# Kernel optimization log

Measured on AMD Instinct MI355X. Metric: run time of the kernel, lower is better.

The kernel has to match this reference:

```python
import jax, jax.numpy as jnp
import numpy as np

NEG_SLOPE = 0.1  # LeakyReLU slope used throughout CamLiFlow

def _batch_gather(feat, idx):
    # feat: [B, C, N], idx: [B, N, K] -> [B, C, N, K]
    return jax.vmap(lambda f, i: f[:, i])(feat, idx)

def _point_conv(xyz, feat, idx, wn_w, wn_b, lin_w, lin_b):
    # xyz: [B,3,N], feat: [B,C,N], idx: [B,N,K]
    B, _, N = xyz.shape
    feat_cat = jnp.concatenate([xyz, feat], axis=1)            # [B, C+3, N]
    knn_xyz = _batch_gather(xyz, idx)                          # [B, 3, N, K]
    rel = knn_xyz - xyz[:, :, :, None]                         # centered neighbor coords
    # weight net: 1x1 conv 3 -> 8 + LeakyReLU
    w = jax.nn.leaky_relu(
        jnp.einsum('oc,bcnk->bonk', wn_w, rel) + wn_b[None, :, None, None],
        NEG_SLOPE)                                             # [B, 8, N, K]
    knn_feat = _batch_gather(feat_cat, idx)                    # [B, C+3, N, K]
    agg = jnp.einsum('bonk,bcnk->bnoc', w, knn_feat)           # [B, N, 8, C+3]
    out = agg.reshape(B, N, -1) @ lin_w.T + lin_b              # [B, N, out]
    return jax.nn.leaky_relu(out, NEG_SLOPE).transpose(0, 2, 1)  # [B, out, N]

def _conv1d(x, w, b):
    # 1x1 Conv1d: x [B,C,N], w [O,C], b [O]
    return jnp.einsum('oc,bcn->bon', w, x) + b[None, :, None]

def setup_inputs() -> dict:
    key = jax.random.key(0)
    ks = jax.random.split(key, 16)
    B, N, K = 4, 8192, 16
    C0, C1, C2, C3 = 128, 128, 128, 64
    s = 0.02
    inp = {
        'xyz': jax.random.normal(ks[0], (B, 3, N), jnp.float32),
        'feat': jax.random.normal(ks[1], (B, C0, N), jnp.float32),
        'knn_indices': jax.random.randint(ks[2], (B, N, K), 0, N),
        # point_conv1
        'wn1_w': jax.random.normal(ks[3], (8, 3), jnp.float32) * s,
        'wn1_b': jnp.zeros((8,), jnp.float32),
        'lin1_w': jax.random.normal(ks[4], (C1, 8 * (C0 + 3)), jnp.float32) * s,
        'lin1_b': jnp.zeros((C1,), jnp.float32),
        # point_conv2
        'wn2_w': jax.random.normal(ks[5], (8, 3), jnp.float32) * s,
        'wn2_b': jnp.zeros((8,), jnp.float32),
        'lin2_w': jax.random.normal(ks[6], (C2, 8 * (C1 + 3)), jnp.float32) * s,
        'lin2_b': jnp.zeros((C2,), jnp.float32),
        # MLP1d: C2 -> C2 -> C3 (1x1 convs + LeakyReLU)
        'm1_w': jax.random.normal(ks[7], (C2, C2), jnp.float32) * s,
        'm1_b': jnp.zeros((C2,), jnp.float32),
        'm2_w': jax.random.normal(ks[8], (C3, C2), jnp.float32) * s,
        'm2_b': jnp.zeros((C3,), jnp.float32),
        # conv_last: C3 -> 3
        'cl_w': jax.random.normal(ks[9], (3, C3), jnp.float32) * s,
        'cl_b': jnp.zeros((3,), jnp.float32),
    }
    return inp

def reference(xyz, feat, knn_indices, wn1_w, wn1_b, lin1_w, lin1_b,
              wn2_w, wn2_b, lin2_w, lin2_b, m1_w, m1_b, m2_w, m2_b,
              cl_w, cl_b):
    f = _point_conv(xyz, feat, knn_indices, wn1_w, wn1_b, lin1_w, lin1_b)  # [B,128,N]
    f = _point_conv(xyz, f, knn_indices, wn2_w, wn2_b, lin2_w, lin2_b)     # [B,128,N]
    f = jax.nn.leaky_relu(_conv1d(f, m1_w, m1_b), NEG_SLOPE)
    flow_feat = jax.nn.leaky_relu(_conv1d(f, m2_w, m2_b), NEG_SLOPE)       # [B,64,N]
    flow = _conv1d(flow_feat, cl_w, cl_b)                                  # [B,3,N]
    return flow_feat, flow
```

## Files before the change

kernel.cpp:

```cpp
#include <hip/hip_runtime.h>

typedef __bf16 bf16x8 __attribute__((ext_vector_type(8)));
typedef float  f32x4  __attribute__((ext_vector_type(4)));
typedef float  f32x2  __attribute__((ext_vector_type(2)));
typedef unsigned int u32x4 __attribute__((ext_vector_type(4)));
typedef unsigned short u16;

#define NPTS 8192
#define NB   4
#define KNN  16
#define ROW  136
#define CF   131
#define JBLK 136
#define NSTEP 34
#define AGG_STRIDE 1096
#define HALF_U16 8704
#define WOFF  17408
#define RBOFF 19456
#define SMEM_U16 19712
#define F2T   0
#define H1OFF 2304
#define FFOFF 4608
#define NEG 0.1f

#define WAITVM(n) __builtin_amdgcn_s_waitcnt(0x0F70 | (n))
#define SB() __builtin_amdgcn_sched_barrier(0)

__device__ __forceinline__ float b2f(u16 h) {
    return __uint_as_float(((unsigned int)h) << 16);
}
__device__ __forceinline__ u16 f2bf(float f) {
    unsigned int u = __float_as_uint(f);
    return (u16)((u + 0x8000u) >> 16);
}
__device__ __forceinline__ void dma16(const u16* g, u16* l) {
    __builtin_amdgcn_global_load_lds(
        (const __attribute__((address_space(1))) void*)g,
        (__attribute__((address_space(3))) void*)l, 16, 0, 0);
}
__device__ __forceinline__ float lrelu(float v) {
    return (v < 0.0f) ? NEG * v : v;
}

__global__ __launch_bounds__(256) void pack_all(
    const float* __restrict__ xyz, const float* __restrict__ feat,
    u16* __restrict__ fcT1, u16* __restrict__ fcT2, float* __restrict__ xyzF,
    const float* __restrict__ l1, const float* __restrict__ l2,
    const float* __restrict__ w1, const float* __restrict__ w2,
    u16* __restrict__ o1, u16* __restrict__ o2,
    u16* __restrict__ o3, u16* __restrict__ o4)
{
    int t = threadIdx.x;
    if (blockIdx.x < 512) {
        __shared__ u16 tile[CF * 65];
        int blk = blockIdx.x;
        int b = blk >> 7;
        int n0 = (blk & 127) << 6;
        int nn = t & 63;
        #pragma unroll 1
        for (int c = (t >> 6); c < CF; c += 4) {
            float v;
            if (c < 3) v = xyz[(size_t)b * 3 * NPTS + (size_t)c * NPTS + n0 + nn];
            else       v = feat[(size_t)b * 128 * NPTS + (size_t)(c - 3) * NPTS + n0 + nn];
            tile[c * 65 + nn] = f2bf(v);
            if (c < 3) xyzF[((size_t)b * NPTS + n0 + nn) * 4 + c] = v;
        }
        __syncthreads();
        #pragma unroll 1
        for (int e = t; e < 64 * ROW; e += 256) {
            int r = e / ROW;
            int c = e - r * ROW;
            u16 v = (c < CF) ? tile[c * 65 + r] : (u16)0;
            size_t row = (size_t)b * NPTS + n0 + r;
            fcT1[row * ROW + c] = v;
            if (c < 3 || c >= CF) fcT2[row * ROW + c] = v;
        }
    } else {
        int blk = blockIdx.x - 512;
        const float* w; u16* out; int O, Cin, remap, b0;
        if (blk < 68)       { w = l1; out = o1; O = 128; Cin = 1048; remap = 1; b0 = 0; }
        else if (blk < 136) { w = l2; out = o2; O = 128; Cin = 1048; remap = 1; b0 = 68; }
        else if (blk < 144) { w = w1; out = o3; O = 128; Cin = 128;  remap = 0; b0 = 136; }
        else                { w = w2; out = o4; O = 64;  Cin = 128;  remap = 0; b0 = 144; }
        int T = O >> 4;
        int tid = (blk - b0) * 256 + t;
        int l = tid & 63;
        int st = tid >> 6;
        int tt = st % T;
        int s = st / T;
        int o = tt * 16 + (l & 15);
        int kb = s * 32 + ((l >> 4) * 8);
        #pragma unroll 1
        for (int j = 0; j < 8; j++) {
            int kh = kb + j;
            u16 v = 0;
            if (remap) {
                int jj = kh / JBLK, cc = kh - jj * JBLK;
                if (cc < CF) v = f2bf(w[(size_t)o * Cin + jj * CF + cc]);
            } else {
                if (kh < Cin) v = f2bf(w[(size_t)o * Cin + kh]);
            }
            out[(size_t)tid * 8 + j] = v;
        }
    }
}

__device__ __forceinline__ void pc_core(
    u16* __restrict__ smem,
    const u16* __restrict__ fcT, const float* __restrict__ xyzF,
    const int* __restrict__ knn, const float* __restrict__ wn_w,
    const float* __restrict__ wn_b, const u16* __restrict__ lwP,
    int pt0, int b, int n0, f32x4& acc1o, f32x4& acc2o)
{
    int t = threadIdx.x;
    int wv = t >> 6, lane = t & 63;
    int p = t >> 4, cl = t & 15;
    u16* rb16 = smem + RBOFF;

    {
        size_t rowC = (size_t)b * NPTS + n0 + p;
        int idxv = knn[rowC * KNN + cl];
        int rb = b * NPTS + idxv;
        rb16[p * 16 + cl] = (u16)rb;
        f32x4 cx = *(const f32x4*)(xyzF + rowC * 4);
        f32x4 nx = *(const f32x4*)(xyzF + (size_t)rb * 4);
        float rx = nx[0] - cx[0], ry = nx[1] - cx[1], rz = nx[2] - cx[2];
        unsigned int wp[4];
        #pragma unroll
        for (int jj = 0; jj < 4; jj++) {
            float a0 = lrelu(wn_w[(2 * jj) * 3 + 0] * rx + wn_w[(2 * jj) * 3 + 1] * ry +
                             wn_w[(2 * jj) * 3 + 2] * rz + wn_b[2 * jj]);
            float a1 = lrelu(wn_w[(2 * jj + 1) * 3 + 0] * rx + wn_w[(2 * jj + 1) * 3 + 1] * ry +
                             wn_w[(2 * jj + 1) * 3 + 2] * rz + wn_b[2 * jj + 1]);
            wp[jj] = (unsigned)f2bf(a0) | ((unsigned)f2bf(a1) << 16);
        }
        *(u32x4*)(smem + WOFF + (p * 16 + cl) * 8) = (u32x4){wp[0], wp[1], wp[2], wp[3]};
    }

    f32x2 acc[4][8];
    float acct[8];
    #pragma unroll
    for (int i = 0; i < 4; i++)
        #pragma unroll
        for (int j = 0; j < 8; j++) acc[i][j] = (f32x2){0.f, 0.f};
    #pragma unroll
    for (int j = 0; j < 8; j++) acct[j] = 0.f;

    int rbidx[5], remu[5], ldso[5];
    #pragma unroll
    for (int i = 0; i < 5; i++) {
        int slot = i * 64 + lane;
        int rl = slot / 17;
        int rem = slot - rl * 17;
        int pp = wv * 4 + (rl >> 2);
        int kk = rl & 3;
        rbidx[i] = pp * 16 + kk;
        remu[i] = rem * 8;
        ldso[i] = (pp * 4 + kk) * 136 + rem * 8;
    }

    auto issue = [&](int c) {
        int h = c & 1;
        #pragma unroll
        for (int i = 0; i < 5; i++) {
            if (i < 4 || lane < 16) {
                int rb = (int)rb16[rbidx[i] + c * 4];
                dma16(fcT + (size_t)rb * ROW + remu[i],
                      smem + h * HALF_U16 + ldso[i]);
            }
        }
    };
    auto consume = [&](int c) {
        int h = c & 1;
        const u16* rpb = smem + h * HALF_U16 + p * (4 * 136);
        const u16* wpb = smem + WOFF + (p * 16 + c * 4) * 8;
        #pragma unroll 2
        for (int kk = 0; kk < 4; kk++) {
            u32x4 rv = *(const u32x4*)(rpb + kk * 136 + cl * 8);
            float tl = (cl < 3) ? b2f(rpb[kk * 136 + 128 + cl]) : 0.0f;
            u32x4 wv4 = *(const u32x4*)(wpb + kk * 8);
            f32x2 v[4];
            float wr[8];
            #pragma unroll
            for (int i = 0; i < 4; i++) {
                unsigned int u = rv[i];
                v[i] = (f32x2){__uint_as_float(u << 16),
                               __uint_as_float(u & 0xFFFF0000u)};
                unsigned int uw = wv4[i];
                wr[2 * i]     = __uint_as_float(uw << 16);
                wr[2 * i + 1] = __uint_as_float(uw & 0xFFFF0000u);
            }
            #pragma unroll
            for (int j = 0; j < 8; j++) {
                f32x2 w2 = (f32x2){wr[j], wr[j]};
                #pragma unroll
                for (int i = 0; i < 4; i++) acc[i][j] += v[i] * w2;
                acct[j] += tl * wr[j];
            }
        }
    };

    issue(0); issue(1);
    #pragma unroll 1
    for (int c = 0; c < 2; c++) {
        WAITVM(5); SB(); consume(c); SB(); issue(c + 2); SB();
    }
    WAITVM(5); SB(); consume(2); SB();
    WAITVM(0); SB(); consume(3);
    __syncthreads();

    {
        #pragma unroll
        for (int j = 0; j < 8; j++) {
            unsigned int o[4];
            #pragma unroll
            for (int i = 0; i < 4; i++) {
                unsigned int lo = f2bf(acc[i][j].x);
                unsigned int hi = f2bf(acc[i][j].y);
                o[i] = lo | (hi << 16);
            }
            *(u32x4*)(smem + p * AGG_STRIDE + j * JBLK + cl * 8) =
                (u32x4){o[0], o[1], o[2], o[3]};
        }
        if (cl < 3) {
            #pragma unroll
            for (int j = 0; j < 8; j++)
                smem[p * AGG_STRIDE + j * JBLK + 128 + cl] = f2bf(acct[j]);
        }
        if (cl < 5) {
            #pragma unroll
            for (int j = 0; j < 8; j++)
                smem[p * AGG_STRIDE + j * JBLK + CF + cl] = 0;
        }
    }
    __syncthreads();

    {
        int m = lane & 15, quad = lane >> 4;
        f32x4 a1 = {0.f, 0.f, 0.f, 0.f};
        f32x4 a2 = {0.f, 0.f, 0.f, 0.f};
        #pragma unroll 4
        for (int s = 0; s < NSTEP; s++) {
            u32x4 av = *(const u32x4*)(smem + m * AGG_STRIDE + s * 32 + quad * 8);
            u32x4 bv1 = *(const u32x4*)(lwP + (((size_t)(s * 8 + wv) * 64 + lane) << 3));
            u32x4 bv2 = *(const u32x4*)(lwP + (((size_t)(s * 8 + wv + 4) * 64 + lane) << 3));
            a1 = __builtin_amdgcn_mfma_f32_16x16x32_bf16(
                __builtin_bit_cast(bf16x8, av), __builtin_bit_cast(bf16x8, bv1), a1, 0, 0, 0);
            a2 = __builtin_amdgcn_mfma_f32_16x16x32_bf16(
                __builtin_bit_cast(bf16x8, av), __builtin_bit_cast(bf16x8, bv2), a2, 0, 0, 0);
        }
        acc1o = a1; acc2o = a2;
    }
}

__global__ __launch_bounds__(256) void pc_kernel0(
    const u16* __restrict__ fcT, const float* __restrict__ xyzF,
    const int* __restrict__ knn, const float* __restrict__ wn_w,
    const float* __restrict__ wn_b, const u16* __restrict__ lwP,
    const float* __restrict__ lin_b, u16* __restrict__ out)
{
    __shared__ __align__(16) u16 smem[SMEM_U16];
    int t = threadIdx.x;
    int wv = t >> 6, lane = t & 63;
    int pt0 = blockIdx.x * 16;
    int b = pt0 >> 13;
    int n0 = pt0 & (NPTS - 1);
    f32x4 a1, a2;
    pc_core(smem, fcT, xyzF, knn, wn_w, wn_b, lwP, pt0, b, n0, a1, a2);
    int col = lane & 15, quad = lane >> 4;
    int o1 = wv * 16 + col, o2 = (wv + 4) * 16 + col;
    float bb1 = lin_b[o1], bb2 = lin_b[o2];
    #pragma unroll
    for (int r = 0; r < 4; r++) {
        int prow = pt0 + quad * 4 + r;
        out[(size_t)prow * ROW + 3 + o1] = f2bf(lrelu(a1[r] + bb1));
        out[(size_t)prow * ROW + 3 + o2] = f2bf(lrelu(a2[r] + bb2));
    }
}

__global__ __launch_bounds__(256) void pc_kernel1(
    const u16* __restrict__ fcT, const float* __restrict__ xyzF,
    const int* __restrict__ knn, const float* __restrict__ wn_w,
    const float* __restrict__ wn_b, const u16* __restrict__ lwP,
    const float* __restrict__ lin_b,
    const u16* __restrict__ m1P, const float* __restrict__ m1_b,
    const u16* __restrict__ m2P, const float* __restrict__ m2_b,
    const float* __restrict__ cl_w, const float* __restrict__ cl_b,
    float* __restrict__ dout)
{
    __shared__ __align__(16) u16 smem[SMEM_U16];
    int t = threadIdx.x;
    int wv = t >> 6, lane = t & 63;
    int pt0 = blockIdx.x * 16;
    int b = pt0 >> 13;
    int n0 = pt0 & (NPTS - 1);
    f32x4 a1, a2;
    pc_core(smem, fcT, xyzF, knn, wn_w, wn_b, lwP, pt0, b, n0, a1, a2);
    int col = lane & 15, quad = lane >> 4;
    int m = lane & 15;

    {
        int o1 = wv * 16 + col, o2 = (wv + 4) * 16 + col;
        float bb1 = lin_b[o1], bb2 = lin_b[o2];
        __syncthreads();
        #pragma unroll
        for (int r = 0; r < 4; r++) {
            int pr = quad * 4 + r;
            smem[F2T + pr * 128 + o1] = f2bf(lrelu(a1[r] + bb1));
            smem[F2T + pr * 128 + o2] = f2bf(lrelu(a2[r] + bb2));
        }
    }
    __syncthreads();

    {
        f32x4 g1 = {0.f, 0.f, 0.f, 0.f};
        f32x4 g2 = {0.f, 0.f, 0.f, 0.f};
        #pragma unroll 2
        for (int s = 0; s < 4; s++) {
            u32x4 av = *(const u32x4*)(smem + F2T + m * 128 + s * 32 + quad * 8);
            u32x4 bv1 = *(const u32x4*)(m1P + (((size_t)(s * 8 + wv) * 64 + lane) << 3));
            u32x4 bv2 = *(const u32x4*)(m1P + (((size_t)(s * 8 + wv + 4) * 64 + lane) << 3));
            g1 = __builtin_amdgcn_mfma_f32_16x16x32_bf16(
                __builtin_bit_cast(bf16x8, av), __builtin_bit_cast(bf16x8, bv1), g1, 0, 0, 0);
            g2 = __builtin_amdgcn_mfma_f32_16x16x32_bf16(
                __builtin_bit_cast(bf16x8, av), __builtin_bit_cast(bf16x8, bv2), g2, 0, 0, 0);
        }
        int o1 = wv * 16 + col, o2 = (wv + 4) * 16 + col;
        float bb1 = m1_b[o1], bb2 = m1_b[o2];
        #pragma unroll
        for (int r = 0; r < 4; r++) {
            int pr = quad * 4 + r;
            smem[H1OFF + pr * 136 + o1] = f2bf(lrelu(g1[r] + bb1));
            smem[H1OFF + pr * 136 + o2] = f2bf(lrelu(g2[r] + bb2));
        }
    }
    __syncthreads();

    {
        float* ffp = (float*)(smem + FFOFF);
        f32x4 g = {0.f, 0.f, 0.f, 0.f};
        #pragma unroll 2
        for (int s = 0; s < 4; s++) {
            u32x4 av = *(const u32x4*)(smem + H1OFF + m * 136 + s * 32 + quad * 8);
            u32x4 bv = *(const u32x4*)(m2P + (((size_t)(s * 4 + wv) * 64 + lane) << 3));
            g = __builtin_amdgcn_mfma_f32_16x16x32_bf16(
                __builtin_bit_cast(bf16x8, av), __builtin_bit_cast(bf16x8, bv), g, 0, 0, 0);
        }
        int o = wv * 16 + col;
        float bb = m2_b[o];
        #pragma unroll
        for (int r = 0; r < 4; r++) {
            int pr = quad * 4 + r;
            float v = lrelu(g[r] + bb);
            dout[((size_t)b * 64 + o) * NPTS + n0 + pr] = v;
            ffp[pr * 68 + o] = v;
        }
    }
    __syncthreads();

    if (t < 48) {
        float* ffp = (float*)(smem + FFOFF);
        int pp = t & 15, oo = t >> 4;
        float a = cl_b[oo];
        #pragma unroll 8
        for (int i = 0; i < 64; i++)
            a += cl_w[oo * 64 + i] * ffp[pp * 68 + i];
        dout[(size_t)NB * 64 * NPTS + ((size_t)b * 3 + oo) * NPTS + n0 + pp] = a;
    }
}

extern "C" void kernel_launch(void* const* d_in, const int* in_sizes, int n_in,
                              void* d_out, int out_size, void* d_ws, size_t ws_size,
                              hipStream_t stream) {
    const float* xyz   = (const float*)d_in[0];
    const float* feat  = (const float*)d_in[1];
    const int*   knn   = (const int*)d_in[2];
    const float* wn1_w = (const float*)d_in[3];
    const float* wn1_b = (const float*)d_in[4];
    const float* lin1w = (const float*)d_in[5];
    const float* lin1b = (const float*)d_in[6];
    const float* wn2_w = (const float*)d_in[7];
    const float* wn2_b = (const float*)d_in[8];
    const float* lin2w = (const float*)d_in[9];
    const float* lin2b = (const float*)d_in[10];
    const float* m1_w  = (const float*)d_in[11];
    const float* m1_b  = (const float*)d_in[12];
    const float* m2_w  = (const float*)d_in[13];
    const float* m2_b  = (const float*)d_in[14];
    const float* cl_w  = (const float*)d_in[15];
    const float* cl_b  = (const float*)d_in[16];
    float* out = (float*)d_out;

    char* ws = (char*)d_ws;
    const size_t BN = (size_t)NB * NPTS;
    u16*   fcT1 = (u16*)(ws);
    u16*   fcT2 = (u16*)(ws + 8912896);
    float* xyzF = (float*)(ws + 17825792);
    u16*   lw1P = (u16*)(ws + 18350080);
    u16*   lw2P = (u16*)(ws + 18628608);
    u16*   m1P  = (u16*)(ws + 18907136);
    u16*   m2P  = (u16*)(ws + 18939904);

    (void)in_sizes; (void)n_in; (void)out_size; (void)ws_size;

    pack_all<<<dim3(660), dim3(256), 0, stream>>>(
        xyz, feat, fcT1, fcT2, xyzF,
        lin1w, lin2w, m1_w, m2_w, lw1P, lw2P, m1P, m2P);
    pc_kernel0<<<dim3(BN / 16), dim3(256), 0, stream>>>(
        fcT1, xyzF, knn, wn1_w, wn1_b, lw1P, lin1b, fcT2);
    pc_kernel1<<<dim3(BN / 16), dim3(256), 0, stream>>>(
        fcT2, xyzF, knn, wn2_w, wn2_b, lw2P, lin2b,
        m1P, m1_b, m2P, m2_b, cl_w, cl_b, out);
}
```

Baseline: 194.3 us.

## Shrink LDS footprint with c-major aggregate layout and chunked staging

Reorders the aggregated K dimension from j-major (136-padded blocks per weight channel) to channel-major interleaved (c*8+j), with the packed linear weights remapped to match. The aggregate is written to LDS in four 32-channel groups plus a tail, each followed by the MFMA steps for that slice, instead of staging the full 16x1096 tile at once. Neighbor gather chunks shrink from 4 to 2 neighbors with 8 pipeline stages, which halves the double buffer. Together these roughly halve shared memory per block, likely to raise occupancy, at the cost of several extra __syncthreads in the projection phase. The F2T row stride is also padded to 136 to reduce bank conflicts.

```diff
diff --git a/kernel.cpp b/kernel.cpp
--- a/kernel.cpp
+++ b/kernel.cpp
@@ -11,13 +11,12 @@
 #define KNN  16
 #define ROW  136
 #define CF   131
-#define JBLK 136
 #define NSTEP 34
-#define AGG_STRIDE 1096
-#define HALF_U16 8704
-#define WOFF  17408
-#define RBOFF 19456
-#define SMEM_U16 19712
+#define HALF_U16 4352
+#define WOFF  8704
+#define RBOFF 10752
+#define SMEM_U16 11008
+#define AGB_STRIDE 264
 #define F2T   0
 #define H1OFF 2304
 #define FFOFF 4608
@@ -95,7 +94,7 @@
             int kh = kb + j;
             u16 v = 0;
             if (remap) {
-                int jj = kh / JBLK, cc = kh - jj * JBLK;
+                int cc = kh >> 3, jj = kh & 7;
                 if (cc < CF) v = f2bf(w[(size_t)o * Cin + jj * CF + cc]);
             } else {
                 if (kh < Cin) v = f2bf(w[(size_t)o * Cin + kh]);
@@ -146,36 +145,37 @@
     #pragma unroll
     for (int j = 0; j < 8; j++) acct[j] = 0.f;
 
-    int rbidx[5], remu[5], ldso[5];
+    int rbidx[3], remu[3], ldso[3];
     #pragma unroll
-    for (int i = 0; i < 5; i++) {
+    for (int i = 0; i < 3; i++) {
         int slot = i * 64 + lane;
         int rl = slot / 17;
         int rem = slot - rl * 17;
-        int pp = wv * 4 + (rl >> 2);
-        int kk = rl & 3;
+        int pp = wv * 4 + (rl >> 1);
+        int kk = rl & 1;
         rbidx[i] = pp * 16 + kk;
         remu[i] = rem * 8;
-        ldso[i] = (pp * 4 + kk) * 136 + rem * 8;
+        ldso[i] = wv * 1088 + rl * 136 + rem * 8;
     }
 
     auto issue = [&](int c) {
         int h = c & 1;
         #pragma unroll
-        for (int i = 0; i < 5; i++) {
-            if (i < 4 || lane < 16) {
-                int rb = (int)rb16[rbidx[i] + c * 4];
+        for (int i = 0; i < 3; i++) {
+            if (i < 2 || lane < 8) {
+                int rb = (int)rb16[rbidx[i] + c * 2];
                 dma16(fcT + (size_t)rb * ROW + remu[i],
                       smem + h * HALF_U16 + ldso[i]);
             }
         }
     };
+
     auto consume = [&](int c) {
         int h = c & 1;
-        const u16* rpb = smem + h * HALF_U16 + p * (4 * 136);
-        const u16* wpb = smem + WOFF + (p * 16 + c * 4) * 8;
-        #pragma unroll 2
-        for (int kk = 0; kk < 4; kk++) {
+        const u16* rpb = smem + h * HALF_U16 + p * 272;
+        const u16* wpb = smem + WOFF + (p * 16 + c * 2) * 8;
+        #pragma unroll
+        for (int kk = 0; kk < 2; kk++) {
             u32x4 rv = *(const u32x4*)(rpb + kk * 136 + cl * 8);
             float tl = (cl < 3) ? b2f(rpb[kk * 136 + 128 + cl]) : 0.0f;
             u32x4 wv4 = *(const u32x4*)(wpb + kk * 8);
@@ -202,46 +202,67 @@
 
     issue(0); issue(1);
     #pragma unroll 1
-    for (int c = 0; c < 2; c++) {
-        WAITVM(5); SB(); consume(c); SB(); issue(c + 2); SB();
-    }
-    WAITVM(5); SB(); consume(2); SB();
-    WAITVM(0); SB(); consume(3);
-    __syncthreads();
-
-    {
-        #pragma unroll
-        for (int j = 0; j < 8; j++) {
-            unsigned int o[4];
-            #pragma unroll
-            for (int i = 0; i < 4; i++) {
-                unsigned int lo = f2bf(acc[i][j].x);
-                unsigned int hi = f2bf(acc[i][j].y);
-                o[i] = lo | (hi << 16);
-            }
-            *(u32x4*)(smem + p * AGG_STRIDE + j * JBLK + cl * 8) =
-                (u32x4){o[0], o[1], o[2], o[3]};
-        }
-        if (cl < 3) {
-            #pragma unroll
-            for (int j = 0; j < 8; j++)
-                smem[p * AGG_STRIDE + j * JBLK + 128 + cl] = f2bf(acct[j]);
-        }
-        if (cl < 5) {
-            #pragma unroll
-            for (int j = 0; j < 8; j++)
-                smem[p * AGG_STRIDE + j * JBLK + CF + cl] = 0;
-        }
-    }
+    for (int c = 0; c < 6; c++) {
+        WAITVM(3); SB(); consume(c); SB(); issue(c + 2); SB();
+    }
+    WAITVM(3); SB(); consume(6); SB();
+    WAITVM(0); SB(); consume(7);
     __syncthreads();
 
     {
         int m = lane & 15, quad = lane >> 4;
+        int myg = cl >> 2, cl4 = cl & 3;
         f32x4 a1 = {0.f, 0.f, 0.f, 0.f};
         f32x4 a2 = {0.f, 0.f, 0.f, 0.f};
-        #pragma unroll 4
-        for (int s = 0; s < NSTEP; s++) {
-            u32x4 av = *(const u32x4*)(smem + m * AGG_STRIDE + s * 32 + quad * 8);
+        #pragma unroll 1
+        for (int g = 0; g < 4; g++) {
+            if (myg == g) {
+                #pragma unroll
+                for (int i = 0; i < 4; i++) {
+                    u32x4 vx = (u32x4){
+                        (unsigned)f2bf(acc[i][0].x) | ((unsigned)f2bf(acc[i][1].x) << 16),
+                        (unsigned)f2bf(acc[i][2].x) | ((unsigned)f2bf(acc[i][3].x) << 16),
+                        (unsigned)f2bf(acc[i][4].x) | ((unsigned)f2bf(acc[i][5].x) << 16),
+                        (unsigned)f2bf(acc[i][6].x) | ((unsigned)f2bf(acc[i][7].x) << 16)};
+                    u32x4 vy = (u32x4){
+                        (unsigned)f2bf(acc[i][0].y) | ((unsigned)f2bf(acc[i][1].y) << 16),
+                        (unsigned)f2bf(acc[i][2].y) | ((unsigned)f2bf(acc[i][3].y) << 16),
+                        (unsigned)f2bf(acc[i][4].y) | ((unsigned)f2bf(acc[i][5].y) << 16),
+                        (unsigned)f2bf(acc[i][6].y) | ((unsigned)f2bf(acc[i][7].y) << 16)};
+                    *(u32x4*)(smem + p * AGB_STRIDE + (cl4 * 8 + 2 * i) * 8) = vx;
+                    *(u32x4*)(smem + p * AGB_STRIDE + (cl4 * 8 + 2 * i + 1) * 8) = vy;
+                }
+            }
+            __syncthreads();
+            #pragma unroll 4
+            for (int sl = 0; sl < 8; sl++) {
+                int s = g * 8 + sl;
+                u32x4 av = *(const u32x4*)(smem + m * AGB_STRIDE + sl * 32 + quad * 8);
+                u32x4 bv1 = *(const u32x4*)(lwP + (((size_t)(s * 8 + wv) * 64 + lane) << 3));
+                u32x4 bv2 = *(const u32x4*)(lwP + (((size_t)(s * 8 + wv + 4) * 64 + lane) << 3));
+                a1 = __builtin_amdgcn_mfma_f32_16x16x32_bf16(
+                    __builtin_bit_cast(bf16x8, av), __builtin_bit_cast(bf16x8, bv1), a1, 0, 0, 0);
+                a2 = __builtin_amdgcn_mfma_f32_16x16x32_bf16(
+                    __builtin_bit_cast(bf16x8, av), __builtin_bit_cast(bf16x8, bv2), a2, 0, 0, 0);
+            }
+            __syncthreads();
+        }
+        if (cl < 8) {
+            u32x4 z = (u32x4){0u, 0u, 0u, 0u};
+            if (cl < 3) {
+                z = (u32x4){
+                    (unsigned)f2bf(acct[0]) | ((unsigned)f2bf(acct[1]) << 16),
+                    (unsigned)f2bf(acct[2]) | ((unsigned)f2bf(acct[3]) << 16),
+                    (unsigned)f2bf(acct[4]) | ((unsigned)f2bf(acct[5]) << 16),
+                    (unsigned)f2bf(acct[6]) | ((unsigned)f2bf(acct[7]) << 16)};
+            }
+            *(u32x4*)(smem + p * AGB_STRIDE + cl * 8) = z;
+        }
+        __syncthreads();
+        #pragma unroll
+        for (int sl = 0; sl < 2; sl++) {
+            int s = 32 + sl;
+            u32x4 av = *(const u32x4*)(smem + m * AGB_STRIDE + sl * 32 + quad * 8);
             u32x4 bv1 = *(const u32x4*)(lwP + (((size_t)(s * 8 + wv) * 64 + lane) << 3));
             u32x4 bv2 = *(const u32x4*)(lwP + (((size_t)(s * 8 + wv + 4) * 64 + lane) << 3));
             a1 = __builtin_amdgcn_mfma_f32_16x16x32_bf16(
@@ -306,8 +327,8 @@
         #pragma unroll
         for (int r = 0; r < 4; r++) {
             int pr = quad * 4 + r;
-            smem[F2T + pr * 128 + o1] = f2bf(lrelu(a1[r] + bb1));
-            smem[F2T + pr * 128 + o2] = f2bf(lrelu(a2[r] + bb2));
+            smem[F2T + pr * 136 + o1] = f2bf(lrelu(a1[r] + bb1));
+            smem[F2T + pr * 136 + o2] = f2bf(lrelu(a2[r] + bb2));
         }
     }
     __syncthreads();
@@ -317,7 +338,7 @@
         f32x4 g2 = {0.f, 0.f, 0.f, 0.f};
         #pragma unroll 2
         for (int s = 0; s < 4; s++) {
-            u32x4 av = *(const u32x4*)(smem + F2T + m * 128 + s * 32 + quad * 8);
+            u32x4 av = *(const u32x4*)(smem + F2T + m * 136 + s * 32 + quad * 8);
             u32x4 bv1 = *(const u32x4*)(m1P + (((size_t)(s * 8 + wv) * 64 + lane) << 3));
             u32x4 bv2 = *(const u32x4*)(m1P + (((size_t)(s * 8 + wv + 4) * 64 + lane) << 3));
             g1 = __builtin_amdgcn_mfma_f32_16x16x32_bf16(
```

After: 250.1 us. 28.7% more time.
